# Kernel tuning notes

Hardware: AMD Instinct MI355X
Metric: run time of the kernel (lower is better)

Reference implementation:

```python
import jax, jax.numpy as jnp
import numpy as np
from jax import lax

DIM = 256
HEADS = 8
WIN = 5
B, H, W = 4, 120, 120


def _templates():
    neg = -0.5
    pos = 1.0 + 1.0 / 3.0
    nor = -3.0 / 8.0
    cnor = 4.0
    nws = [
        [[nor, nor, nor], [nor, cnor, nor], [nor, nor, nor]],
        [[neg, pos, neg], [neg, pos, neg], [neg, pos, neg]],
        [[neg, neg, neg], [pos, pos, pos], [neg, neg, neg]],
        [[pos, neg, neg], [neg, pos, neg], [neg, neg, pos]],
        [[neg, neg, pos], [neg, pos, neg], [pos, neg, neg]],
        [[neg, pos, neg], [pos, pos, neg], [neg, neg, neg]],
        [[neg, pos, neg], [neg, pos, pos], [neg, neg, neg]],
        [[neg, neg, neg], [pos, pos, neg], [neg, pos, neg]],
        [[neg, neg, neg], [neg, pos, pos], [neg, pos, neg]],
    ]
    return np.asarray(nws, dtype=np.float32)  # [9,3,3]


def setup_inputs() -> dict:
    key = jax.random.key(0)
    kx, kk, kv, kq, ko = jax.random.split(key, 5)
    x = jax.random.normal(kx, (B, DIM, H, W), dtype=jnp.float32)
    # depthwise conv templates, tiled per channel: [9, DIM, 1, 3, 3]
    nws = _templates()
    conv_w = jnp.asarray(np.tile(nws[:, None, None, :, :], (1, DIM, 1, 1, 1)))
    s = DIM ** -0.5
    Wk = jax.random.normal(kk, (DIM, DIM), dtype=jnp.float32) * s
    Wv = jax.random.normal(kv, (DIM, DIM), dtype=jnp.float32) * s
    Wq = jax.random.normal(kq, (DIM, DIM), dtype=jnp.float32) * s
    Wout = jax.random.normal(ko, (DIM, DIM), dtype=jnp.float32) * s
    bout = jnp.zeros((DIM,), dtype=jnp.float32)
    return {"x": x, "conv_w": conv_w, "Wk": Wk, "Wv": Wv, "Wq": Wq,
            "Wout": Wout, "bout": bout}


def reference(x, conv_w, Wk, Wv, Wq, Wout, bout):
    b, c, h, w = x.shape
    num = conv_w.shape[0]
    win, heads = WIN, HEADS
    dh = c // heads
    scale = dh ** -0.5
    b1, b2 = h // win, w // win

    # 9 depthwise 3x3 convs (padding=1), concatenated on channel dim
    kvs = [lax.conv_general_dilated(x, conv_w[i], (1, 1), "SAME",
                                    feature_group_count=c)
           for i in range(num)]
    pm = jnp.concatenate(kvs, axis=1)  # [b, num*c, h, w]

    kv0 = pm.reshape(b, num, c, b1, win, b2, win)
    kv0 = kv0.transpose(0, 3, 5, 1, 4, 6, 2).reshape(b * b1 * b2, num * win * win, c)
    q0 = x.reshape(b, c, b1, win, b2, win)
    q0 = q0.transpose(0, 2, 4, 3, 5, 1).reshape(b * b1 * b2, win * win, c)

    def heads_split(t):  # [B_, n, c] -> [B_, heads, n, dh]
        return t.reshape(t.shape[0], t.shape[1], heads, dh).transpose(0, 2, 1, 3)

    kh = heads_split(kv0 @ Wk.T)
    vh = heads_split(kv0 @ Wv.T)
    qh = heads_split(q0 @ Wq.T) * scale

    attn = jax.nn.softmax(jnp.einsum("bhqd,bhkd->bhqk", qh, kh), axis=-1)
    out = jnp.einsum("bhqk,bhkd->bhqd", attn, vh)          # [B_, heads, 25, dh]
    out = out.transpose(0, 2, 1, 3).reshape(b * b1 * b2, win * win, c)
    out = out @ Wout.T + bout

    # window merge back to NCHW
    out = out.reshape(b, b1, b2, win, win, c)
    out = out.transpose(0, 5, 1, 3, 2, 4).reshape(b, c, h, w)
    return out
```

## Files before the change

kernel.cpp:

```cpp
#include <hip/hip_runtime.h>

#define IMGW 120
#define IMGH 120
#define NPIX 14400
#define XS   460800

typedef unsigned short u16;
typedef short bf16x8 __attribute__((ext_vector_type(8)));
typedef float f32x4 __attribute__((ext_vector_type(4)));

__device__ inline u16 f2bf(float f) {
  unsigned int x = __float_as_uint(f);
  unsigned int r = x + 0x7FFFu + ((x >> 16) & 1u);
  return (u16)(r >> 16);
}
__device__ inline unsigned int pk2(float a, float b) {
  return (unsigned int)f2bf(a) | ((unsigned int)f2bf(b) << 16);
}
__device__ inline float bf2f(u16 h) { return __uint_as_float(((unsigned int)h) << 16); }

__global__ __launch_bounds__(256) void wconv_kernel(
    const float* __restrict__ Wq, const float* __restrict__ Wk,
    const float* __restrict__ Wv, const float* __restrict__ Wo,
    u16* __restrict__ Wb)
{
  const int t = threadIdx.x, bx = blockIdx.x, mat = blockIdx.y;
  const float* src = mat == 0 ? Wq : mat == 1 ? Wk : mat == 2 ? Wv : Wo;
  const float sc = (mat == 0) ? 0.17677669529663687f : 1.0f;
  const int e0 = (bx * 256 + t) * 4;
  float4 v = *(const float4*)(src + e0);
  uint2 u;
  u.x = pk2(v.x * sc, v.y * sc);
  u.y = pk2(v.z * sc, v.w * sc);
  *(uint2*)(Wb + (size_t)mat * 65536 + e0) = u;
}

__global__ __launch_bounds__(256) void xpose_kernel(
    const float* __restrict__ x, u16* __restrict__ x_t)
{
  __shared__ u16 sh[64 * 66];
  const int t = threadIdx.x;
  const int p0 = blockIdx.x * 64;
  const int b  = blockIdx.y;
  const int c0 = blockIdx.z * 64;
  const float* xb = x + ((size_t)b * 256 + c0) * NPIX + p0;
  #pragma unroll
  for (int it = 0; it < 16; ++it) {
    int ch = it * 4 + (t >> 6), pix = t & 63;
    sh[pix * 66 + ch] = f2bf(xb[(size_t)ch * NPIX + pix]);
  }
  __syncthreads();
  u16* ob = x_t + ((size_t)b * NPIX + p0) * 256 + c0;
  const unsigned int* sh32 = (const unsigned int*)sh;
  #pragma unroll
  for (int it = 0; it < 8; ++it) {
    int flat = it * 256 + t;
    int pix = flat >> 5, c2 = flat & 31;
    ((unsigned int*)(ob + (size_t)pix * 256))[c2] = sh32[pix * 33 + c2];
  }
}

__global__ __launch_bounds__(256) void projmm_kernel(
    const u16* __restrict__ x_t, const u16* __restrict__ Wb,
    u16* __restrict__ Qb, u16* __restrict__ Kb, u16* __restrict__ Vb)
{
  __shared__ u16 Ws[256 * 40];
  __shared__ u16 Xs[64 * 40];
  const int t = threadIdx.x;
  const int lane = t & 63, wv = t >> 6;
  const int p0 = blockIdx.x * 64;
  const int b  = blockIdx.y;
  const int mat = blockIdx.z;

  const u16* Wm = Wb + (size_t)mat * 65536;
  const u16* Xb = x_t + ((size_t)b * NPIX + p0) * 256;

  f32x4 acc[4][4];
  #pragma unroll
  for (int i = 0; i < 4; ++i)
    #pragma unroll
    for (int j = 0; j < 4; ++j) acc[i][j] = {0.f, 0.f, 0.f, 0.f};

  for (int kk = 0; kk < 8; ++kk) {
    #pragma unroll
    for (int p = 0; p < 4; ++p) {
      int fl = t + 256 * p;
      int d = fl >> 2, c = fl & 3;
      uint4 u = *(const uint4*)(Wm + d * 256 + kk * 32 + c * 8);
      *(uint4*)&Ws[d * 40 + c * 8] = u;
    }
    {
      int pix = t >> 2, c = t & 3;
      uint4 u = *(const uint4*)(Xb + (size_t)pix * 256 + kk * 32 + c * 8);
      *(uint4*)&Xs[pix * 40 + c * 8] = u;
    }
    __syncthreads();
    bf16x8 af[4], bfr[4];
    #pragma unroll
    for (int f = 0; f < 4; ++f)
      af[f] = *(const bf16x8*)&Ws[(wv * 64 + f * 16 + (lane & 15)) * 40 + (lane >> 4) * 8];
    #pragma unroll
    for (int f = 0; f < 4; ++f)
      bfr[f] = *(const bf16x8*)&Xs[(f * 16 + (lane & 15)) * 40 + (lane >> 4) * 8];
    #pragma unroll
    for (int df = 0; df < 4; ++df)
      #pragma unroll
      for (int pf = 0; pf < 4; ++pf)
        acc[df][pf] = __builtin_amdgcn_mfma_f32_16x16x32_bf16(af[df], bfr[pf], acc[df][pf], 0, 0, 0);
    __syncthreads();
  }

  u16* O = (mat == 0) ? Qb : (mat == 1) ? Kb : Vb;
  #pragma unroll
  for (int df = 0; df < 4; ++df) {
    int dim0 = wv * 64 + df * 16 + (lane >> 4) * 4;
    int h = dim0 >> 5, dl0 = dim0 & 31;
    #pragma unroll
    for (int pf = 0; pf < 4; ++pf) {
      int pix = p0 + pf * 16 + (lane & 15);
      f32x4 v = acc[df][pf];
      uint2 u;
      u.x = pk2(v[0], v[1]);
      u.y = pk2(v[2], v[3]);
      *(uint2*)&O[((size_t)(b * 8 + h) * NPIX + pix) * 32 + dl0] = u;
    }
  }
}

__global__ __launch_bounds__(64, 3) void attn_kernel(
    const u16* __restrict__ Qb,
    const u16* __restrict__ Kb,
    const u16* __restrict__ Vb,
    u16* __restrict__ AO)
{
  __shared__ __align__(16) unsigned char smem[13440];
  float* SA   = (float*)smem;
  u16*   vsT  = (u16*)(smem + 8704);
  float* drow = (float*)(smem + 13312);

  const int lane = threadIdx.x;
  const int bid = blockIdx.x;
  const int h = bid / 2304;
  const int w = bid % 2304;
  const int b = w / 576;
  const int rr = w % 576;
  const int by = rr / 24, bx = rr % 24;
  const int y0 = by * 5, x0 = bx * 5;
  const size_t gbase = (size_t)(b * 8 + h) * XS;
  const u16* Qg = Qb + gbase;
  const u16* Kg = Kb + gbase;
  const u16* Vg = Vb + gbase;

  const int cc = lane & 15, kgrp = lane >> 4;
  const int ks8 = kgrp * 8;
  const int r0 = kgrp * 4;
  const int kpl = lane & 31;

  bf16x8 aq0, aq1;
  {
    int rA = cc;
    int wyA = (rA * 13) >> 6, wxA = rA - wyA * 5;
    uint4 uA = *(const uint4*)(Qg + (size_t)((y0 + wyA) * IMGW + x0 + wxA) * 32 + ks8);
    aq0 = *(bf16x8*)&uA;
    int rB = cc + 16; int rBc = rB < 25 ? rB : 0;
    int wyB = (rBc * 13) >> 6, wxB = rBc - wyB * 5;
    uint4 uB = *(const uint4*)(Qg + (size_t)((y0 + wyB) * IMGW + x0 + wxB) * 32 + ks8);
    aq1 = *(bf16x8*)&uB;
  }

  bf16x8 bk[4];
  #pragma unroll
  for (int nt = 0; nt < 4; ++nt) {
    int pp = cc + nt * 16;
    int hy = (pp * 37) >> 8, hx = pp - hy * 7;
    int gy = y0 - 1 + hy, gx = x0 - 1 + hx;
    bool inb = (gy >= 0) && (gy < IMGH) && (gx >= 0) && (gx < IMGW);
    int gyc = min(max(gy, 0), IMGH - 1), gxc = min(max(gx, 0), IMGW - 1);
    uint4 u = *(const uint4*)(Kg + (size_t)(gyc * IMGW + gxc) * 32 + ks8);
    if (pp < 49 && !inb) u = make_uint4(0u, 0u, 0u, 0u);
    bk[nt] = *(bf16x8*)&u;
  }

  #pragma unroll
  for (int it = 0; it < 4; ++it) {
    int f = lane + 64 * it;
    int pp = f >> 2, c = f & 3;
    int hy = (pp * 37) >> 8, hx = pp - hy * 7;
    int gy = y0 - 1 + hy, gx = x0 - 1 + hx;
    uint4 u = make_uint4(0u, 0u, 0u, 0u);
    if (pp < 49 && gy >= 0 && gy < IMGH && gx >= 0 && gx < IMGW)
      u = *(const uint4*)(Vg + (size_t)(gy * IMGW + gx) * 32 + c * 8);
    const int d0 = c * 8;
    vsT[(d0 + 0) * 72 + pp] = (u16)(u.x & 0xffff);
    vsT[(d0 + 1) * 72 + pp] = (u16)(u.x >> 16);
    vsT[(d0 + 2) * 72 + pp] = (u16)(u.y & 0xffff);
    vsT[(d0 + 3) * 72 + pp] = (u16)(u.y >> 16);
    vsT[(d0 + 4) * 72 + pp] = (u16)(u.z & 0xffff);
    vsT[(d0 + 5) * 72 + pp] = (u16)(u.z >> 16);
    vsT[(d0 + 6) * 72 + pp] = (u16)(u.w & 0xffff);
    vsT[(d0 + 7) * 72 + pp] = (u16)(u.w >> 16);
  }

  {
    const f32x4 z = {0.f, 0.f, 0.f, 0.f};
    f32x4 s[2][4];
    #pragma unroll
    for (int nt = 0; nt < 4; ++nt) {
      s[0][nt] = __builtin_amdgcn_mfma_f32_16x16x32_bf16(aq0, bk[nt], z, 0, 0, 0);
      s[1][nt] = __builtin_amdgcn_mfma_f32_16x16x32_bf16(aq1, bk[nt], z, 0, 0, 0);
    }
    #pragma unroll
    for (int mt = 0; mt < 2; ++mt)
      #pragma unroll
      for (int nt = 0; nt < 4; ++nt)
        #pragma unroll
        for (int i = 0; i < 4; ++i) {
          int q = mt * 16 + r0 + i, pp = nt * 16 + cc;
          if (q < 25 && pp < 49) SA[q * 68 + pp] = s[mt][nt][i];
        }
  }

  int idxA[9], idxB[9];
  float selA[9], selB[9];
  {
    const int hb = lane & 32;
    const int ppA = kpl, ppB = 32 + kpl;
    const int hyA = (ppA * 37) >> 8, hxA = ppA - hyA * 7;
    const int hyB = (ppB * 37) >> 8, hxB = ppB - hyB * 7;
    #pragma unroll
    for (int dy = 0; dy < 3; ++dy)
      #pragma unroll
      for (int dx = 0; dx < 3; ++dx) {
        int j = dy * 3 + dx;
        int kyA = hyA - dy, kxA = hxA - dx;
        bool vA = ((unsigned)kyA < 5u) && ((unsigned)kxA < 5u);
        idxA[j] = (hb + (vA ? kyA * 5 + kxA : 0)) << 2;
        selA[j] = vA ? 1.f : 0.f;
        int kyB = hyB - dy, kxB = hxB - dx;
        bool vB = ((unsigned)kyB < 5u) && ((unsigned)kxB < 5u);
        idxB[j] = (hb + (vB ? kyB * 5 + kxB : 0)) << 2;
        selB[j] = vB ? 1.f : 0.f;
      }
  }

  const float DPN = 11.f / 6.f;
  const float LOG2E = 1.44269504f;
  const int kyq = (kpl * 13) >> 6, kxq = kpl - kyq * 5;
  const int sboff = kyq * 7 + kxq;

  for (int t = 0; t < 13; ++t) {
    const int q = 2 * t + (lane >> 5);
    const bool act = (kpl < 25) && (q < 25);
    const float* sp = SA + q * 68 + sboff;
    float s0 = sp[0], s1 = sp[1], s2 = sp[2];
    float s3 = sp[7], s4 = sp[8], s5 = sp[9];
    float s6 = sp[14], s7 = sp[15], s8 = sp[16];

    float st = ((s0 + s1) + (s2 + s3)) + ((s5 + s6) + (s7 + s8)) + s4;
    float l0 = -0.375f * st + 4.375f * s4;
    float base = -0.5f * st + DPN * s4;
    float l1 = base + DPN * (s1 + s7);
    float l2 = base + DPN * (s3 + s5);
    float l3 = base + DPN * (s0 + s8);
    float l4 = base + DPN * (s2 + s6);
    float l5 = base + DPN * (s1 + s3);
    float l6 = base + DPN * (s1 + s5);
    float l7 = base + DPN * (s3 + s7);
    float l8 = base + DPN * (s5 + s7);

    float p0 = exp2f(fmaf(l0, LOG2E, -32.f));
    float p1 = exp2f(fmaf(l1, LOG2E, -32.f));
    float p2 = exp2f(fmaf(l2, LOG2E, -32.f));
    float p3 = exp2f(fmaf(l3, LOG2E, -32.f));
    float p4 = exp2f(fmaf(l4, LOG2E, -32.f));
    float p5 = exp2f(fmaf(l5, LOG2E, -32.f));
    float p6 = exp2f(fmaf(l6, LOG2E, -32.f));
    float p7 = exp2f(fmaf(l7, LOG2E, -32.f));
    float p8 = exp2f(fmaf(l8, LOG2E, -32.f));
    float ps = ((p0 + p1) + (p2 + p3)) + ((p4 + p5) + (p6 + p7)) + p8;

    float sv = act ? ps : 0.f;
    sv += __int_as_float(__builtin_amdgcn_update_dpp(0, __float_as_int(sv), 0xB1, 0xF, 0xF, true));
    sv += __int_as_float(__builtin_amdgcn_update_dpp(0, __float_as_int(sv), 0x4E, 0xF, 0xF, true));
    sv += __shfl_xor(sv, 4);
    sv += __shfl_xor(sv, 8);
    sv += __shfl_xor(sv, 16);
    if (kpl == 0 && q < 25) drow[q] = __builtin_amdgcn_rcpf(sv + 1e-35f);

    float psm0 = ps - p0;
    float basec = -0.5f * psm0 - 0.375f * p0;
    float cv[9];
    cv[0] = basec + DPN * p3;
    cv[1] = basec + DPN * ((p1 + p5) + p6);
    cv[2] = basec + DPN * p4;
    cv[3] = basec + DPN * ((p2 + p5) + p7);
    cv[4] = 4.f * p0 + (4.f / 3.f) * psm0;
    cv[5] = basec + DPN * ((p2 + p6) + p8);
    cv[6] = basec + DPN * p4;
    cv[7] = basec + DPN * ((p1 + p7) + p8);
    cv[8] = basec + DPN * p3;

    float a = 0.f, a2 = 0.f;
    #pragma unroll
    for (int j = 0; j < 9; ++j) {
      int cj = __float_as_int(cv[j]);
      a  = fmaf(selA[j], __int_as_float(__builtin_amdgcn_ds_bpermute(idxA[j], cj)), a);
      a2 = fmaf(selB[j], __int_as_float(__builtin_amdgcn_ds_bpermute(idxB[j], cj)), a2);
    }

    if (q < 25) {
      u16* arow = (u16*)((char*)SA + q * 272);
      u16 h1 = f2bf(a);
      arow[kpl]      = h1;
      arow[64 + kpl] = f2bf(a - bf2f(h1));
      u16 h2 = f2bf(a2);
      arow[32 + kpl] = h2;
      arow[96 + kpl] = f2bf(a2 - bf2f(h2));
    }
  }

  __syncthreads();

  {
    f32x4 o[2][2];
    #pragma unroll
    for (int i = 0; i < 2; ++i)
      #pragma unroll
      for (int j = 0; j < 2; ++j) o[i][j] = {0.f, 0.f, 0.f, 0.f};
    #pragma unroll
    for (int kx = 0; kx < 2; ++kx) {
      const int koff = kx * 64 + kgrp * 16;
      const char* sa = (const char*)SA;
      bf16x8 ah0 = *(const bf16x8*)(sa + cc * 272 + koff);
      bf16x8 ah1 = *(const bf16x8*)(sa + (cc + 16) * 272 + koff);
      bf16x8 al0 = *(const bf16x8*)(sa + cc * 272 + 128 + koff);
      bf16x8 al1 = *(const bf16x8*)(sa + (cc + 16) * 272 + 128 + koff);
      bf16x8 b0  = *(const bf16x8*)&vsT[cc * 72 + kx * 32 + ks8];
      bf16x8 b1  = *(const bf16x8*)&vsT[(cc + 16) * 72 + kx * 32 + ks8];
      o[0][0] = __builtin_amdgcn_mfma_f32_16x16x32_bf16(ah0, b0, o[0][0], 0, 0, 0);
      o[0][0] = __builtin_amdgcn_mfma_f32_16x16x32_bf16(al0, b0, o[0][0], 0, 0, 0);
      o[0][1] = __builtin_amdgcn_mfma_f32_16x16x32_bf16(ah0, b1, o[0][1], 0, 0, 0);
      o[0][1] = __builtin_amdgcn_mfma_f32_16x16x32_bf16(al0, b1, o[0][1], 0, 0, 0);
      o[1][0] = __builtin_amdgcn_mfma_f32_16x16x32_bf16(ah1, b0, o[1][0], 0, 0, 0);
      o[1][0] = __builtin_amdgcn_mfma_f32_16x16x32_bf16(al1, b0, o[1][0], 0, 0, 0);
      o[1][1] = __builtin_amdgcn_mfma_f32_16x16x32_bf16(ah1, b1, o[1][1], 0, 0, 0);
      o[1][1] = __builtin_amdgcn_mfma_f32_16x16x32_bf16(al1, b1, o[1][1], 0, 0, 0);
    }
    #pragma unroll
    for (int mt = 0; mt < 2; ++mt) {
      float4 rv = *(const float4*)&drow[mt * 16 + r0];
      #pragma unroll
      for (int i = 0; i < 4; ++i) {
        int q = mt * 16 + r0 + i;
        if (q < 25) {
          int qy = (q * 13) >> 6, qx = q - qy * 5;
          u16* dst = AO + gbase + ((size_t)((y0 + qy) * IMGW + x0 + qx)) * 32;
          float r = (&rv.x)[i];
          dst[cc]      = f2bf(o[mt][0][i] * r);
          dst[cc + 16] = f2bf(o[mt][1][i] * r);
        }
      }
    }
  }
}

__global__ __launch_bounds__(256) void outmm_kernel(
    const u16* __restrict__ AOb, const u16* __restrict__ Wb,
    const float* __restrict__ bout, float* __restrict__ O)
{
  __shared__ u16 Ws[256 * 40];
  __shared__ u16 Xs[64 * 40];
  const int t = threadIdx.x;
  const int lane = t & 63, wv = t >> 6;
  const int p0 = blockIdx.x * 64;
  const int b  = blockIdx.y;
  const u16* Wm = Wb + (size_t)3 * 65536;

  f32x4 acc[4][4];
  #pragma unroll
  for (int i = 0; i < 4; ++i)
    #pragma unroll
    for (int j = 0; j < 4; ++j) acc[i][j] = {0.f, 0.f, 0.f, 0.f};

  for (int kk = 0; kk < 8; ++kk) {
    #pragma unroll
    for (int p = 0; p < 4; ++p) {
      int fl = t + 256 * p;
      int d = fl >> 2, c = fl & 3;
      uint4 u = *(const uint4*)(Wm + d * 256 + kk * 32 + c * 8);
      *(uint4*)&Ws[d * 40 + c * 8] = u;
    }
    {
      int pix = t >> 2, c = t & 3;
      uint4 u = *(const uint4*)(AOb + ((size_t)(b * 8 + kk) * NPIX + p0 + pix) * 32 + c * 8);
      *(uint4*)&Xs[pix * 40 + c * 8] = u;
    }
    __syncthreads();
    bf16x8 af[4], bfr[4];
    #pragma unroll
    for (int f = 0; f < 4; ++f)
      af[f] = *(const bf16x8*)&Ws[(wv * 64 + f * 16 + (lane & 15)) * 40 + (lane >> 4) * 8];
    #pragma unroll
    for (int f = 0; f < 4; ++f)
      bfr[f] = *(const bf16x8*)&Xs[(f * 16 + (lane & 15)) * 40 + (lane >> 4) * 8];
    #pragma unroll
    for (int df = 0; df < 4; ++df)
      #pragma unroll
      for (int pf = 0; pf < 4; ++pf)
        acc[df][pf] = __builtin_amdgcn_mfma_f32_16x16x32_bf16(af[df], bfr[pf], acc[df][pf], 0, 0, 0);
    __syncthreads();
  }

  #pragma unroll
  for (int df = 0; df < 4; ++df) {
    int dim0 = wv * 64 + df * 16 + (lane >> 4) * 4;
    float4 bv = *(const float4*)&bout[dim0];
    #pragma unroll
    for (int pf = 0; pf < 4; ++pf) {
      int pix = p0 + pf * 16 + (lane & 15);
      f32x4 v = acc[df][pf];
      float* ob = O + (size_t)b * 256 * NPIX + pix;
      ob[(size_t)(dim0 + 0) * NPIX] = v[0] + bv.x;
      ob[(size_t)(dim0 + 1) * NPIX] = v[1] + bv.y;
      ob[(size_t)(dim0 + 2) * NPIX] = v[2] + bv.z;
      ob[(size_t)(dim0 + 3) * NPIX] = v[3] + bv.w;
    }
  }
}

extern "C" void kernel_launch(void* const* d_in, const int* in_sizes, int n_in,
                              void* d_out, int out_size, void* d_ws, size_t ws_size,
                              hipStream_t stream) {
  const float* x    = (const float*)d_in[0];
  const float* Wk   = (const float*)d_in[2];
  const float* Wv   = (const float*)d_in[3];
  const float* Wq   = (const float*)d_in[4];
  const float* Wout = (const float*)d_in[5];
  const float* bout = (const float*)d_in[6];

  u16* x_t = (u16*)d_out;
  u16* Qb  = x_t + (size_t)4 * NPIX * 256;
  u16* Kb  = (u16*)d_ws;
  u16* Vb  = Kb + (size_t)4 * NPIX * 256;
  u16* AOb = Vb + (size_t)4 * NPIX * 256;
  u16* Wb  = AOb + (size_t)4 * NPIX * 256;

  wconv_kernel<<<dim3(64, 4), 256, 0, stream>>>(Wq, Wk, Wv, Wout, Wb);
  xpose_kernel<<<dim3(225, 4, 4), 256, 0, stream>>>(x, x_t);
  projmm_kernel<<<dim3(225, 4, 3), 256, 0, stream>>>(x_t, Wb, Qb, Kb, Vb);
  attn_kernel<<<dim3(18432), 64, 0, stream>>>(Qb, Kb, Vb, AOb);
  outmm_kernel<<<dim3(225, 4), 256, 0, stream>>>(AOb, Wb, bout, (float*)d_out);
}
```

Baseline: 221.5 us.

## Process two attention windows per wavefront block in attn_kernel

Each 64-thread attention block now handles two (head, window) pairs instead of one, halving the grid and issuing both windows' Q/K/V loads up front for more memory-level parallelism. Shared memory is doubled and restructured per window, with the softmax reciprocal stored in the padding of each score row rather than a separate array. The softmax/conv loop interleaves both windows, raising ILP at the cost of higher register and LDS use and dropping the occupancy hint from launch bounds.

```diff
diff --git a/kernel.cpp b/kernel.cpp
--- a/kernel.cpp
+++ b/kernel.cpp
@@ -127,87 +127,101 @@
   }
 }
 
-__global__ __launch_bounds__(64, 3) void attn_kernel(
+__global__ __launch_bounds__(64) void attn_kernel(
     const u16* __restrict__ Qb,
     const u16* __restrict__ Kb,
     const u16* __restrict__ Vb,
     u16* __restrict__ AO)
 {
-  __shared__ __align__(16) unsigned char smem[13440];
-  float* SA   = (float*)smem;
-  u16*   vsT  = (u16*)(smem + 8704);
-  float* drow = (float*)(smem + 13312);
+  __shared__ __align__(16) unsigned char smem[2 * 11408];
 
   const int lane = threadIdx.x;
   const int bid = blockIdx.x;
-  const int h = bid / 2304;
-  const int w = bid % 2304;
-  const int b = w / 576;
-  const int rr = w % 576;
-  const int by = rr / 24, bx = rr % 24;
-  const int y0 = by * 5, x0 = bx * 5;
-  const size_t gbase = (size_t)(b * 8 + h) * XS;
-  const u16* Qg = Qb + gbase;
-  const u16* Kg = Kb + gbase;
-  const u16* Vg = Vb + gbase;
 
   const int cc = lane & 15, kgrp = lane >> 4;
   const int ks8 = kgrp * 8;
   const int r0 = kgrp * 4;
   const int kpl = lane & 31;
 
-  bf16x8 aq0, aq1;
-  {
+  size_t gbase[2];
+  int y0s[2], x0s[2];
+  #pragma unroll
+  for (int s = 0; s < 2; ++s) {
+    int wh = bid * 2 + s;
+    int h = wh / 2304;
+    int w = wh % 2304;
+    int b = w / 576;
+    int rr2 = w % 576;
+    int by = rr2 / 24, bx = rr2 % 24;
+    y0s[s] = by * 5; x0s[s] = bx * 5;
+    gbase[s] = (size_t)(b * 8 + h) * XS;
+  }
+
+  bf16x8 aq0[2], aq1[2];
+  #pragma unroll
+  for (int s = 0; s < 2; ++s) {
+    const u16* Qg = Qb + gbase[s];
     int rA = cc;
     int wyA = (rA * 13) >> 6, wxA = rA - wyA * 5;
-    uint4 uA = *(const uint4*)(Qg + (size_t)((y0 + wyA) * IMGW + x0 + wxA) * 32 + ks8);
-    aq0 = *(bf16x8*)&uA;
+    uint4 uA = *(const uint4*)(Qg + (size_t)((y0s[s] + wyA) * IMGW + x0s[s] + wxA) * 32 + ks8);
+    aq0[s] = *(bf16x8*)&uA;
     int rB = cc + 16; int rBc = rB < 25 ? rB : 0;
     int wyB = (rBc * 13) >> 6, wxB = rBc - wyB * 5;
-    uint4 uB = *(const uint4*)(Qg + (size_t)((y0 + wyB) * IMGW + x0 + wxB) * 32 + ks8);
-    aq1 = *(bf16x8*)&uB;
-  }
-
-  bf16x8 bk[4];
-  #pragma unroll
-  for (int nt = 0; nt < 4; ++nt) {
-    int pp = cc + nt * 16;
-    int hy = (pp * 37) >> 8, hx = pp - hy * 7;
-    int gy = y0 - 1 + hy, gx = x0 - 1 + hx;
-    bool inb = (gy >= 0) && (gy < IMGH) && (gx >= 0) && (gx < IMGW);
-    int gyc = min(max(gy, 0), IMGH - 1), gxc = min(max(gx, 0), IMGW - 1);
-    uint4 u = *(const uint4*)(Kg + (size_t)(gyc * IMGW + gxc) * 32 + ks8);
-    if (pp < 49 && !inb) u = make_uint4(0u, 0u, 0u, 0u);
-    bk[nt] = *(bf16x8*)&u;
-  }
-
-  #pragma unroll
-  for (int it = 0; it < 4; ++it) {
-    int f = lane + 64 * it;
-    int pp = f >> 2, c = f & 3;
-    int hy = (pp * 37) >> 8, hx = pp - hy * 7;
-    int gy = y0 - 1 + hy, gx = x0 - 1 + hx;
-    uint4 u = make_uint4(0u, 0u, 0u, 0u);
-    if (pp < 49 && gy >= 0 && gy < IMGH && gx >= 0 && gx < IMGW)
-      u = *(const uint4*)(Vg + (size_t)(gy * IMGW + gx) * 32 + c * 8);
-    const int d0 = c * 8;
-    vsT[(d0 + 0) * 72 + pp] = (u16)(u.x & 0xffff);
-    vsT[(d0 + 1) * 72 + pp] = (u16)(u.x >> 16);
-    vsT[(d0 + 2) * 72 + pp] = (u16)(u.y & 0xffff);
-    vsT[(d0 + 3) * 72 + pp] = (u16)(u.y >> 16);
-    vsT[(d0 + 4) * 72 + pp] = (u16)(u.z & 0xffff);
-    vsT[(d0 + 5) * 72 + pp] = (u16)(u.z >> 16);
-    vsT[(d0 + 6) * 72 + pp] = (u16)(u.w & 0xffff);
-    vsT[(d0 + 7) * 72 + pp] = (u16)(u.w >> 16);
-  }
-
-  {
+    uint4 uB = *(const uint4*)(Qg + (size_t)((y0s[s] + wyB) * IMGW + x0s[s] + wxB) * 32 + ks8);
+    aq1[s] = *(bf16x8*)&uB;
+  }
+
+  bf16x8 bk[2][4];
+  #pragma unroll
+  for (int s = 0; s < 2; ++s) {
+    const u16* Kg = Kb + gbase[s];
+    #pragma unroll
+    for (int nt = 0; nt < 4; ++nt) {
+      int pp = cc + nt * 16;
+      int hy = (pp * 37) >> 8, hx = pp - hy * 7;
+      int gy = y0s[s] - 1 + hy, gx = x0s[s] - 1 + hx;
+      bool inb = (gy >= 0) && (gy < IMGH) && (gx >= 0) && (gx < IMGW);
+      int gyc = min(max(gy, 0), IMGH - 1), gxc = min(max(gx, 0), IMGW - 1);
+      uint4 u = *(const uint4*)(Kg + (size_t)(gyc * IMGW + gxc) * 32 + ks8);
+      if (pp < 49 && !inb) u = make_uint4(0u, 0u, 0u, 0u);
+      bk[s][nt] = *(bf16x8*)&u;
+    }
+  }
+
+  #pragma unroll
+  for (int s = 0; s < 2; ++s) {
+    const u16* Vg = Vb + gbase[s];
+    u16* vsT = (u16*)(smem + s * 11408 + 6800);
+    #pragma unroll
+    for (int it = 0; it < 4; ++it) {
+      int f = lane + 64 * it;
+      int pp = f >> 2, c = f & 3;
+      int hy = (pp * 37) >> 8, hx = pp - hy * 7;
+      int gy = y0s[s] - 1 + hy, gx = x0s[s] - 1 + hx;
+      uint4 u = make_uint4(0u, 0u, 0u, 0u);
+      if (pp < 49 && gy >= 0 && gy < IMGH && gx >= 0 && gx < IMGW)
+        u = *(const uint4*)(Vg + (size_t)(gy * IMGW + gx) * 32 + c * 8);
+      const int d0 = c * 8;
+      vsT[(d0 + 0) * 72 + pp] = (u16)(u.x & 0xffff);
+      vsT[(d0 + 1) * 72 + pp] = (u16)(u.x >> 16);
+      vsT[(d0 + 2) * 72 + pp] = (u16)(u.y & 0xffff);
+      vsT[(d0 + 3) * 72 + pp] = (u16)(u.y >> 16);
+      vsT[(d0 + 4) * 72 + pp] = (u16)(u.z & 0xffff);
+      vsT[(d0 + 5) * 72 + pp] = (u16)(u.z >> 16);
+      vsT[(d0 + 6) * 72 + pp] = (u16)(u.w & 0xffff);
+      vsT[(d0 + 7) * 72 + pp] = (u16)(u.w >> 16);
+    }
+  }
+
+  #pragma unroll
+  for (int s = 0; s < 2; ++s) {
+    float* SA = (float*)(smem + s * 11408);
     const f32x4 z = {0.f, 0.f, 0.f, 0.f};
-    f32x4 s[2][4];
+    f32x4 sacc[2][4];
     #pragma unroll
     for (int nt = 0; nt < 4; ++nt) {
-      s[0][nt] = __builtin_amdgcn_mfma_f32_16x16x32_bf16(aq0, bk[nt], z, 0, 0, 0);
-      s[1][nt] = __builtin_amdgcn_mfma_f32_16x16x32_bf16(aq1, bk[nt], z, 0, 0, 0);
+      sacc[0][nt] = __builtin_amdgcn_mfma_f32_16x16x32_bf16(aq0[s], bk[s][nt], z, 0, 0, 0);
+      sacc[1][nt] = __builtin_amdgcn_mfma_f32_16x16x32_bf16(aq1[s], bk[s][nt], z, 0, 0, 0);
     }
     #pragma unroll
     for (int mt = 0; mt < 2; ++mt)
@@ -216,7 +230,7 @@
         #pragma unroll
         for (int i = 0; i < 4; ++i) {
           int q = mt * 16 + r0 + i, pp = nt * 16 + cc;
-          if (q < 25 && pp < 49) SA[q * 68 + pp] = s[mt][nt][i];
+          if (q < 25 && pp < 49) SA[q * 68 + pp] = sacc[mt][nt][i];
         }
   }
 
@@ -251,77 +265,86 @@
   for (int t = 0; t < 13; ++t) {
     const int q = 2 * t + (lane >> 5);
     const bool act = (kpl < 25) && (q < 25);
-    const float* sp = SA + q * 68 + sboff;
-    float s0 = sp[0], s1 = sp[1], s2 = sp[2];
-    float s3 = sp[7], s4 = sp[8], s5 = sp[9];
-    float s6 = sp[14], s7 = sp[15], s8 = sp[16];
-
-    float st = ((s0 + s1) + (s2 + s3)) + ((s5 + s6) + (s7 + s8)) + s4;
-    float l0 = -0.375f * st + 4.375f * s4;
-    float base = -0.5f * st + DPN * s4;
-    float l1 = base + DPN * (s1 + s7);
-    float l2 = base + DPN * (s3 + s5);
-    float l3 = base + DPN * (s0 + s8);
-    float l4 = base + DPN * (s2 + s6);
-    float l5 = base + DPN * (s1 + s3);
-    float l6 = base + DPN * (s1 + s5);
-    float l7 = base + DPN * (s3 + s7);
-    float l8 = base + DPN * (s5 + s7);
-
-    float p0 = exp2f(fmaf(l0, LOG2E, -32.f));
-    float p1 = exp2f(fmaf(l1, LOG2E, -32.f));
-    float p2 = exp2f(fmaf(l2, LOG2E, -32.f));
-    float p3 = exp2f(fmaf(l3, LOG2E, -32.f));
-    float p4 = exp2f(fmaf(l4, LOG2E, -32.f));
-    float p5 = exp2f(fmaf(l5, LOG2E, -32.f));
-    float p6 = exp2f(fmaf(l6, LOG2E, -32.f));
-    float p7 = exp2f(fmaf(l7, LOG2E, -32.f));
-    float p8 = exp2f(fmaf(l8, LOG2E, -32.f));
-    float ps = ((p0 + p1) + (p2 + p3)) + ((p4 + p5) + (p6 + p7)) + p8;
-
-    float sv = act ? ps : 0.f;
-    sv += __int_as_float(__builtin_amdgcn_update_dpp(0, __float_as_int(sv), 0xB1, 0xF, 0xF, true));
-    sv += __int_as_float(__builtin_amdgcn_update_dpp(0, __float_as_int(sv), 0x4E, 0xF, 0xF, true));
-    sv += __shfl_xor(sv, 4);
-    sv += __shfl_xor(sv, 8);
-    sv += __shfl_xor(sv, 16);
-    if (kpl == 0 && q < 25) drow[q] = __builtin_amdgcn_rcpf(sv + 1e-35f);
-
-    float psm0 = ps - p0;
-    float basec = -0.5f * psm0 - 0.375f * p0;
-    float cv[9];
-    cv[0] = basec + DPN * p3;
-    cv[1] = basec + DPN * ((p1 + p5) + p6);
-    cv[2] = basec + DPN * p4;
-    cv[3] = basec + DPN * ((p2 + p5) + p7);
-    cv[4] = 4.f * p0 + (4.f / 3.f) * psm0;
-    cv[5] = basec + DPN * ((p2 + p6) + p8);
-    cv[6] = basec + DPN * p4;
-    cv[7] = basec + DPN * ((p1 + p7) + p8);
-    cv[8] = basec + DPN * p3;
-
-    float a = 0.f, a2 = 0.f;
-    #pragma unroll
-    for (int j = 0; j < 9; ++j) {
-      int cj = __float_as_int(cv[j]);
-      a  = fmaf(selA[j], __int_as_float(__builtin_amdgcn_ds_bpermute(idxA[j], cj)), a);
-      a2 = fmaf(selB[j], __int_as_float(__builtin_amdgcn_ds_bpermute(idxB[j], cj)), a2);
-    }
-
-    if (q < 25) {
-      u16* arow = (u16*)((char*)SA + q * 272);
-      u16 h1 = f2bf(a);
-      arow[kpl]      = h1;
-      arow[64 + kpl] = f2bf(a - bf2f(h1));
-      u16 h2 = f2bf(a2);
-      arow[32 + kpl] = h2;
-      arow[96 + kpl] = f2bf(a2 - bf2f(h2));
+    #pragma unroll
+    for (int s = 0; s < 2; ++s) {
+      unsigned char* sm = smem + s * 11408;
+      float* SA = (float*)sm;
+      const float* sp = SA + q * 68 + sboff;
+      float s0 = sp[0], s1 = sp[1], s2 = sp[2];
+      float s3 = sp[7], s4 = sp[8], s5 = sp[9];
+      float s6 = sp[14], s7 = sp[15], s8 = sp[16];
+
+      float st = ((s0 + s1) + (s2 + s3)) + ((s5 + s6) + (s7 + s8)) + s4;
+      float l0 = -0.375f * st + 4.375f * s4;
+      float base = -0.5f * st + DPN * s4;
+      float l1 = base + DPN * (s1 + s7);
+      float l2 = base + DPN * (s3 + s5);
+      float l3 = base + DPN * (s0 + s8);
+      float l4 = base + DPN * (s2 + s6);
+      float l5 = base + DPN * (s1 + s3);
+      float l6 = base + DPN * (s1 + s5);
+      float l7 = base + DPN * (s3 + s7);
+      float l8 = base + DPN * (s5 + s7);
+
+      float p0 = exp2f(fmaf(l0, LOG2E, -32.f));
+      float p1 = exp2f(fmaf(l1, LOG2E, -32.f));
+      float p2 = exp2f(fmaf(l2, LOG2E, -32.f));
+      float p3 = exp2f(fmaf(l3, LOG2E, -32.f));
+      float p4 = exp2f(fmaf(l4, LOG2E, -32.f));
+      float p5 = exp2f(fmaf(l5, LOG2E, -32.f));
+      float p6 = exp2f(fmaf(l6, LOG2E, -32.f));
+      float p7 = exp2f(fmaf(l7, LOG2E, -32.f));
+      float p8 = exp2f(fmaf(l8, LOG2E, -32.f));
+      float ps = ((p0 + p1) + (p2 + p3)) + ((p4 + p5) + (p6 + p7)) + p8;
+
+      float sv = act ? ps : 0.f;
+      sv += __int_as_float(__builtin_amdgcn_update_dpp(0, __float_as_int(sv), 0xB1, 0xF, 0xF, true));
+      sv += __int_as_float(__builtin_amdgcn_update_dpp(0, __float_as_int(sv), 0x4E, 0xF, 0xF, true));
+      sv += __shfl_xor(sv, 4);
+      sv += __shfl_xor(sv, 8);
+      sv += __shfl_xor(sv, 16);
+      if (kpl == 0 && q < 25)
+        *(float*)(sm + q * 272 + 256) = __builtin_amdgcn_rcpf(sv + 1e-35f);
+
+      float psm0 = ps - p0;
+      float basec = -0.5f * psm0 - 0.375f * p0;
+      float cv[9];
+      cv[0] = basec + DPN * p3;
+      cv[1] = basec + DPN * ((p1 + p5) + p6);
+      cv[2] = basec + DPN * p4;
+      cv[3] = basec + DPN * ((p2 + p5) + p7);
+      cv[4] = 4.f * p0 + (4.f / 3.f) * psm0;
+      cv[5] = basec + DPN * ((p2 + p6) + p8);
+      cv[6] = basec + DPN * p4;
+      cv[7] = basec + DPN * ((p1 + p7) + p8);
+      cv[8] = basec + DPN * p3;
+
+      float a = 0.f, a2 = 0.f;
+      #pragma unroll
+      for (int j = 0; j < 9; ++j) {
+        int cj = __float_as_int(cv[j]);
+        a  = fmaf(selA[j], __int_as_float(__builtin_amdgcn_ds_bpermute(idxA[j], cj)), a);
+        a2 = fmaf(selB[j], __int_as_float(__builtin_amdgcn_ds_bpermute(idxB[j], cj)), a2);
+      }
+
+      if (q < 25) {
+        u16* arow = (u16*)(sm + q * 272);
+        u16 h1 = f2bf(a);
+        arow[kpl]      = h1;
+        arow[64 + kpl] = f2bf(a - bf2f(h1));
+        u16 h2 = f2bf(a2);
+        arow[32 + kpl] = h2;
+        arow[96 + kpl] = f2bf(a2 - bf2f(h2));
+      }
     }
   }
 
   __syncthreads();
 
-  {
+  #pragma unroll
+  for (int s = 0; s < 2; ++s) {
+    unsigned char* sm = smem + s * 11408;
+    const u16* vsT = (const u16*)(sm + 6800);
     f32x4 o[2][2];
     #pragma unroll
     for (int i = 0; i < 2; ++i)
@@ -330,7 +353,7 @@
     #pragma unroll
     for (int kx = 0; kx < 2; ++kx) {
       const int koff = kx * 64 + kgrp * 16;
-      const char* sa = (const char*)SA;
+      const char* sa = (const char*)sm;
       bf16x8 ah0 = *(const bf16x8*)(sa + cc * 272 + koff);
       bf16x8 ah1 = *(const bf16x8*)(sa + (cc + 16) * 272 + koff);
       bf16x8 al0 = *(const bf16x8*)(sa + cc * 272 + 128 + koff);
@@ -348,14 +371,13 @@
     }
     #pragma unroll
     for (int mt = 0; mt < 2; ++mt) {
-      float4 rv = *(const float4*)&drow[mt * 16 + r0];
       #pragma unroll
       for (int i = 0; i < 4; ++i) {
         int q = mt * 16 + r0 + i;
         if (q < 25) {
+          float r = *(const float*)(sm + q * 272 + 256);
           int qy = (q * 13) >> 6, qx = q - qy * 5;
-          u16* dst = AO + gbase + ((size_t)((y0 + qy) * IMGW + x0 + qx)) * 32;
-          float r = (&rv.x)[i];
+          u16* dst = AO + gbase[s] + ((size_t)((y0s[s] + qy) * IMGW + x0s[s] + qx)) * 32;
           dst[cc]      = f2bf(o[mt][0][i] * r);
           dst[cc + 16] = f2bf(o[mt][1][i] * r);
         }
@@ -448,6 +470,6 @@
   wconv_kernel<<<dim3(64, 4), 256, 0, stream>>>(Wq, Wk, Wv, Wout, Wb);
   xpose_kernel<<<dim3(225, 4, 4), 256, 0, stream>>>(x, x_t);
   projmm_kernel<<<dim3(225, 4, 3), 256, 0, stream>>>(x_t, Wb, Qb, Kb, Vb);
-  attn_kernel<<<dim3(18432), 64, 0, stream>>>(Qb, Kb, Vb, AOb);
+  attn_kernel<<<dim3(9216), 64, 0, stream>>>(Qb, Kb, Vb, AOb);
   outmm_kernel<<<dim3(225, 4), 256, 0, stream>>>(AOb, Wb, bout, (float*)d_out);
 }
```

Result: slower. 258.2 us (+16.6%).
